# Optimization experiments

Hardware: AMD Instinct MI355X
Metric: run time of the kernel (lower is better)

The kernel has to match this reference:

```python
import jax, jax.numpy as jnp
import numpy as np

N = 100000          # nodes
E = 1600000         # edges (avg degree 16)
F_IN = 128          # input node features
H1, C1 = 8, 8       # conv1: 8 heads, 8 channels/head -> 64 concat
NUM_CLASSES = 40    # conv2: 1 head, 40 channels
EPS = 1e-16         # PyG softmax denominator epsilon
NEG_SLOPE = 0.2     # PyG GATConv default leaky_relu slope


def setup_inputs() -> dict:
    key = jax.random.key(0)
    ks = jax.random.split(key, 12)
    x = jax.random.normal(ks[0], (N, F_IN), jnp.float32)
    edge_index = jax.random.randint(ks[1], (2, E), 0, N, dtype=jnp.int64)
    edge_attr = jax.random.normal(ks[2], (E, 1), jnp.float32)
    # layer 1 params (Glorot-ish scaling)
    s1 = 1.0 / np.sqrt(F_IN)
    W1 = jax.random.normal(ks[3], (F_IN, H1 * C1), jnp.float32) * s1
    a_src1 = jax.random.normal(ks[4], (H1, C1), jnp.float32) * (1.0 / np.sqrt(C1))
    a_dst1 = jax.random.normal(ks[5], (H1, C1), jnp.float32) * (1.0 / np.sqrt(C1))
    b1 = jnp.zeros((H1 * C1,), jnp.float32)
    # layer 2 params: in = 64 (conv1 concat output), 1 head, NUM_CLASSES channels
    s2 = 1.0 / np.sqrt(H1 * C1)
    W2 = jax.random.normal(ks[6], (H1 * C1, NUM_CLASSES), jnp.float32) * s2
    a_src2 = jax.random.normal(ks[7], (1, NUM_CLASSES), jnp.float32) * (1.0 / np.sqrt(NUM_CLASSES))
    a_dst2 = jax.random.normal(ks[8], (1, NUM_CLASSES), jnp.float32) * (1.0 / np.sqrt(NUM_CLASSES))
    b2 = jnp.zeros((NUM_CLASSES,), jnp.float32)
    return {"x": x, "edge_index": edge_index, "edge_attr": edge_attr,
            "W1": W1, "a_src1": a_src1, "a_dst1": a_dst1, "b1": b1,
            "W2": W2, "a_src2": a_src2, "a_dst2": a_dst2, "b2": b2}


def gat_conv(x, src, dst, W, a_s, a_d, b, heads, out_ch):
    """PyG GATConv: linear -> per-edge leaky-relu attention -> dst softmax -> scatter-add."""
    n = x.shape[0]
    h = (x @ W).reshape(n, heads, out_ch)                 # [N,H,C]
    alpha_s = jnp.sum(h * a_s, axis=-1)                   # [N,H]
    alpha_d = jnp.sum(h * a_d, axis=-1)                   # [N,H]
    e = jax.nn.leaky_relu(alpha_s[src] + alpha_d[dst], NEG_SLOPE)  # [Etot,H]
    # segment softmax over incoming edges per destination node
    m = jax.ops.segment_max(e, dst, num_segments=n)       # [N,H]
    e = jnp.exp(e - m[dst])
    denom = jax.ops.segment_sum(e, dst, num_segments=n)   # [N,H]
    alpha = e / (denom[dst] + EPS)                        # [Etot,H]
    msg = h[src] * alpha[:, :, None]                      # [Etot,H,C]
    out = jax.ops.segment_sum(msg, dst, num_segments=n)   # [N,H,C]
    return out.reshape(n, heads * out_ch) + b             # concat heads + bias


def reference(x, edge_index, edge_attr, W1, a_src1, a_dst1, b1, W2, a_src2, a_dst2, b2):
    n = x.shape[0]
    # PyG GATConv adds self-loops by default
    loops = jnp.arange(n, dtype=edge_index.dtype)
    src = jnp.concatenate([edge_index[0], loops])
    dst = jnp.concatenate([edge_index[1], loops])
    x = x.astype(jnp.float32)
    x1 = jax.nn.elu(gat_conv(x, src, dst, W1, a_src1, a_dst1, b1, H1, C1))
    x2 = jax.nn.elu(gat_conv(x1, src, dst, W2, a_src2, a_dst2, b2, 1, NUM_CLASSES))
    return x2
```

## Files before the change

### kernel.cpp

```cpp
#include <hip/hip_runtime.h>
#include <math.h>

#define NN 100000
#define NE 1600000
#define NETOT (NE + NN)
#define FIN 128
#define H1N 8
#define D1 64
#define NC 40
#define LNT 64

#define BSH 9
#define BNODES 512
#define NBUC ((NN + BNODES - 1) / BNODES)
#define EPB 4096
#define NBLKA ((NE + EPB - 1) / EPB)
#define BCAP 9216

__device__ __forceinline__ float leakyf(float x) { return x >= 0.0f ? x : 0.2f * x; }
__device__ __forceinline__ float eluf(float x)   { return x > 0.0f ? x : expm1f(x); }

__device__ __forceinline__ unsigned short f2bf(float f) {
  unsigned u = __float_as_uint(f);
  u += 0x7fffu + ((u >> 16) & 1u);
  return (unsigned short)(u >> 16);
}
__device__ __forceinline__ float bf2f(unsigned short s) {
  return __uint_as_float((unsigned)s << 16);
}

__global__ void k_detect(const long long* __restrict__ ei, int* __restrict__ flag) {
  if (blockIdx.x == 0 && threadIdx.x == 0) {
    int is64 = 1;
    for (int i = 0; i < 16; ++i) {
      long long v = ei[i];
      if (v < 0 || v >= NN) is64 = 0;
    }
    *flag = is64;
  }
}

__global__ __launch_bounds__(256) void k_passA(const void* __restrict__ ei,
                        const int* __restrict__ flag,
                        unsigned int* __restrict__ subbuf, int* __restrict__ bcnt) {
  __shared__ unsigned int   pay[EPB];
  __shared__ unsigned short bk[EPB];
  __shared__ unsigned int   spay[EPB];
  __shared__ unsigned short sbk[EPB];
  __shared__ int hist[256];
  __shared__ int lstart[256];
  __shared__ int cur[256];
  __shared__ int gbase[256];
  int t = threadIdx.x;
  int e0 = blockIdx.x * EPB;
  int cnt = min(EPB, NE - e0);
  hist[t] = 0;
  __syncthreads();
  bool f64 = (*flag) != 0;
  for (int i = t; i < cnt; i += 256) {
    int s, d;
    if (f64) {
      const long long* p = (const long long*)ei;
      s = (int)p[e0 + i]; d = (int)p[NE + e0 + i];
    } else {
      const int* p = (const int*)ei;
      s = p[e0 + i]; d = p[NE + e0 + i];
    }
    int b = d >> BSH;
    pay[i] = ((unsigned)s << BSH) | (unsigned)(d & (BNODES - 1));
    bk[i] = (unsigned short)b;
    atomicAdd(&hist[b], 1);
  }
  __syncthreads();
  int v = hist[t];
  lstart[t] = v;
  __syncthreads();
  for (int st = 1; st < 256; st <<= 1) {
    int xv = (t >= st) ? lstart[t - st] : 0;
    __syncthreads();
    lstart[t] += xv;
    __syncthreads();
  }
  int excl = lstart[t] - v;
  __syncthreads();
  lstart[t] = excl;
  cur[t] = excl;
  gbase[t] = (v > 0) ? atomicAdd(&bcnt[t], v) : 0;
  __syncthreads();
  for (int i = t; i < cnt; i += 256) {
    int b = bk[i];
    int pos = atomicAdd(&cur[b], 1);
    spay[pos] = pay[i];
    sbk[pos] = (unsigned short)b;
  }
  __syncthreads();
  for (int i = t; i < cnt; i += 256) {
    int b = sbk[i];
    int o = gbase[b] + (i - lstart[b]);
    if (o < BCAP) subbuf[(size_t)b * BCAP + o] = spay[i];
  }
}

__global__ void k_bucketsum(const int* __restrict__ bcnt, int* __restrict__ bucket_base,
                            int* __restrict__ row_start) {
  __shared__ int sh[256];
  int t = threadIdx.x;
  int tot = 0;
  if (t < NBUC) {
    int d0 = t << BSH;
    int nloc = min(BNODES, NN - d0);
    tot = nloc + min(bcnt[t], BCAP);
  }
  sh[t] = tot;
  __syncthreads();
  for (int s = 1; s < 256; s <<= 1) {
    int x = (t >= s) ? sh[t - s] : 0;
    __syncthreads();
    sh[t] += x;
    __syncthreads();
  }
  if (t < NBUC) bucket_base[t] = sh[t] - tot;
  if (t == NBUC - 1) row_start[NN] = sh[t];
}

__global__ __launch_bounds__(256) void k_passB(const int* __restrict__ bcnt,
                       const unsigned int* __restrict__ subbuf,
                       const int* __restrict__ bucket_base,
                       int* __restrict__ row_start, int* __restrict__ csr) {
  __shared__ int hist[BNODES];
  __shared__ int ps[256];
  __shared__ int cur[BNODES];
  int b = blockIdx.x, t = threadIdx.x;
  int d0 = b << BSH;
  int nloc = min(BNODES, NN - d0);
  hist[t] = 0; hist[t + 256] = 0;
  __syncthreads();
  int cnt = min(bcnt[b], BCAP);
  const unsigned int* sb = subbuf + (size_t)b * BCAP;
  for (int i = t; i < cnt; i += 256)
    atomicAdd(&hist[sb[i] & (BNODES - 1)], 1);
  __syncthreads();
  int j0 = 2 * t, j1 = 2 * t + 1;
  int s0 = (j0 < nloc) ? hist[j0] + 1 : 0;
  int s1 = (j1 < nloc) ? hist[j1] + 1 : 0;
  int pairsum = s0 + s1;
  ps[t] = pairsum;
  __syncthreads();
  for (int s = 1; s < 256; s <<= 1) {
    int x = (t >= s) ? ps[t - s] : 0;
    __syncthreads();
    ps[t] += x;
    __syncthreads();
  }
  int excl = ps[t] - pairsum + bucket_base[b];
  if (j0 < nloc) {
    row_start[d0 + j0] = excl;
    csr[excl] = d0 + j0;
    cur[j0] = excl + 1;
  }
  if (j1 < nloc) {
    int rs = excl + s0;
    row_start[d0 + j1] = rs;
    csr[rs] = d0 + j1;
    cur[j1] = rs + 1;
  }
  __syncthreads();
  for (int i = t; i < cnt; i += 256) {
    unsigned u = sb[i];
    int pos = atomicAdd(&cur[u & (BNODES - 1)], 1);
    csr[pos] = (int)(u >> BSH);
  }
}

#define XS1(node, k) xs[(node) * FIN + ((k) ^ ((node) & 31))]
__global__ void k_lin1(const float* __restrict__ x, const float* __restrict__ W,
                       const float* __restrict__ aw_s, const float* __restrict__ aw_d,
                       unsigned short* __restrict__ h, float* __restrict__ als,
                       float* __restrict__ ald) {
  __shared__ float ws[FIN * D1];
  __shared__ float xs[LNT * FIN];
  int t = threadIdx.x;
  int base = blockIdx.x * LNT;
  for (int i = t; i < FIN * D1; i += 256) ws[i] = W[i];
  for (int i = t; i < LNT * FIN; i += 256) {
    int node = i >> 7, k = i & 127;
    int gn = base + node;
    if (gn >= NN) gn = NN - 1;
    XS1(node, k) = x[(size_t)gn * FIN + k];
  }
  __syncthreads();
  int head = t & 7, ng = t >> 3;
  int n0l = ng * 2, n1l = n0l + 1;
  float acc0[8] = {0, 0, 0, 0, 0, 0, 0, 0};
  float acc1[8] = {0, 0, 0, 0, 0, 0, 0, 0};
  #pragma unroll 4
  for (int k = 0; k < FIN; ++k) {
    float x0 = XS1(n0l, k);
    float x1v = XS1(n1l, k);
    const float4* wr = (const float4*)&ws[k * D1 + head * 8];
    float4 wa = wr[0], wb = wr[1];
    acc0[0] = fmaf(x0, wa.x, acc0[0]); acc1[0] = fmaf(x1v, wa.x, acc1[0]);
    acc0[1] = fmaf(x0, wa.y, acc0[1]); acc1[1] = fmaf(x1v, wa.y, acc1[1]);
    acc0[2] = fmaf(x0, wa.z, acc0[2]); acc1[2] = fmaf(x1v, wa.z, acc1[2]);
    acc0[3] = fmaf(x0, wa.w, acc0[3]); acc1[3] = fmaf(x1v, wa.w, acc1[3]);
    acc0[4] = fmaf(x0, wb.x, acc0[4]); acc1[4] = fmaf(x1v, wb.x, acc1[4]);
    acc0[5] = fmaf(x0, wb.y, acc0[5]); acc1[5] = fmaf(x1v, wb.y, acc1[5]);
    acc0[6] = fmaf(x0, wb.z, acc0[6]); acc1[6] = fmaf(x1v, wb.z, acc1[6]);
    acc0[7] = fmaf(x0, wb.w, acc0[7]); acc1[7] = fmaf(x1v, wb.w, acc1[7]);
  }
  int n0 = base + n0l, n1 = base + n1l;
  float aws[8], awd[8];
  #pragma unroll
  for (int c = 0; c < 8; ++c) { aws[c] = aw_s[head * 8 + c]; awd[c] = aw_d[head * 8 + c]; }
  if (n0 < NN) {
    float s = 0.f, d = 0.f;
    #pragma unroll
    for (int c = 0; c < 8; ++c) {
      h[(size_t)n0 * D1 + head * 8 + c] = f2bf(acc0[c]);
      s = fmaf(acc0[c], aws[c], s);
      d = fmaf(acc0[c], awd[c], d);
    }
    als[n0 * H1N + head] = s;
    ald[n0 * H1N + head] = d;
  }
  if (n1 < NN) {
    float s = 0.f, d = 0.f;
    #pragma unroll
    for (int c = 0; c < 8; ++c) {
      h[(size_t)n1 * D1 + head * 8 + c] = f2bf(acc1[c]);
      s = fmaf(acc1[c], aws[c], s);
      d = fmaf(acc1[c], awd[c], d);
    }
    als[n1 * H1N + head] = s;
    ald[n1 * H1N + head] = d;
  }
}

#define XS2(node, k) xs[(node) * D1 + ((k) ^ ((node) & 31))]
__global__ void k_lin2(const float* __restrict__ x, const float* __restrict__ W,
                       const float* __restrict__ aw_s, const float* __restrict__ aw_d,
                       unsigned short* __restrict__ h, float* __restrict__ als,
                       float* __restrict__ ald) {
  __shared__ float ws[D1 * D1];
  __shared__ float xs[LNT * D1];
  int t = threadIdx.x;
  int base = blockIdx.x * LNT;
  for (int i = t; i < D1 * D1; i += 256) {
    int k = i >> 6, c = i & 63;
    ws[i] = (c < NC) ? W[k * NC + c] : 0.f;
  }
  for (int i = t; i < LNT * D1; i += 256) {
    int node = i >> 6, k = i & 63;
    int gn = base + node;
    if (gn >= NN) gn = NN - 1;
    XS2(node, k) = x[(size_t)gn * D1 + k];
  }
  __syncthreads();
  int g = t & 7, ng = t >> 3;
  int n0l = ng * 2, n1l = n0l + 1;
  float acc0[8] = {0, 0, 0, 0, 0, 0, 0, 0};
  float acc1[8] = {0, 0, 0, 0, 0, 0, 0, 0};
  #pragma unroll 4
  for (int k = 0; k < D1; ++k) {
    float x0 = XS2(n0l, k);
    float x1v = XS2(n1l, k);
    const float4* wr = (const float4*)&ws[k * D1 + g * 8];
    float4 wa = wr[0], wb = wr[1];
    acc0[0] = fmaf(x0, wa.x, acc0[0]); acc1[0] = fmaf(x1v, wa.x, acc1[0]);
    acc0[1] = fmaf(x0, wa.y, acc0[1]); acc1[1] = fmaf(x1v, wa.y, acc1[1]);
    acc0[2] = fmaf(x0, wa.z, acc0[2]); acc1[2] = fmaf(x1v, wa.z, acc1[2]);
    acc0[3] = fmaf(x0, wa.w, acc0[3]); acc1[3] = fmaf(x1v, wa.w, acc1[3]);
    acc0[4] = fmaf(x0, wb.x, acc0[4]); acc1[4] = fmaf(x1v, wb.x, acc1[4]);
    acc0[5] = fmaf(x0, wb.y, acc0[5]); acc1[5] = fmaf(x1v, wb.y, acc1[5]);
    acc0[6] = fmaf(x0, wb.z, acc0[6]); acc1[6] = fmaf(x1v, wb.z, acc1[6]);
    acc0[7] = fmaf(x0, wb.w, acc0[7]); acc1[7] = fmaf(x1v, wb.w, acc1[7]);
  }
  int n0 = base + n0l, n1 = base + n1l;
  float aws[8], awd[8];
  #pragma unroll
  for (int c = 0; c < 8; ++c) {
    int col = g * 8 + c;
    aws[c] = (col < NC) ? aw_s[col] : 0.f;
    awd[c] = (col < NC) ? aw_d[col] : 0.f;
  }
  float s0 = 0.f, d0 = 0.f, s1 = 0.f, d1 = 0.f;
  #pragma unroll
  for (int c = 0; c < 8; ++c) {
    s0 = fmaf(acc0[c], aws[c], s0); d0 = fmaf(acc0[c], awd[c], d0);
    s1 = fmaf(acc1[c], aws[c], s1); d1 = fmaf(acc1[c], awd[c], d1);
  }
  s0 += __shfl_xor(s0, 1); d0 += __shfl_xor(d0, 1); s1 += __shfl_xor(s1, 1); d1 += __shfl_xor(d1, 1);
  s0 += __shfl_xor(s0, 2); d0 += __shfl_xor(d0, 2); s1 += __shfl_xor(s1, 2); d1 += __shfl_xor(d1, 2);
  s0 += __shfl_xor(s0, 4); d0 += __shfl_xor(d0, 4); s1 += __shfl_xor(s1, 4); d1 += __shfl_xor(d1, 4);
  if (n0 < NN && g < 5) {
    #pragma unroll
    for (int c = 0; c < 8; ++c) h[(size_t)n0 * NC + g * 8 + c] = f2bf(acc0[c]);
  }
  if (n1 < NN && g < 5) {
    #pragma unroll
    for (int c = 0; c < 8; ++c) h[(size_t)n1 * NC + g * 8 + c] = f2bf(acc1[c]);
  }
  if (g == 0) {
    if (n0 < NN) { als[n0] = s0; ald[n0] = d0; }
    if (n1 < NN) { als[n1] = s1; ald[n1] = d1; }
  }
}

__global__ void k_node1(const int* __restrict__ row_start, const int* __restrict__ csr,
                        const unsigned short* __restrict__ h, const float* __restrict__ als,
                        const float* __restrict__ ald, const float* __restrict__ b,
                        float* __restrict__ x1) {
  __shared__ float pl[4][64 * 9];
  int wid = threadIdx.x >> 6, lane = threadIdx.x & 63;
  int n = blockIdx.x * 4 + wid;
  if (n >= NN) return;
  float* pw = pl[wid];
  int r0 = row_start[n], r1 = row_start[n + 1];
  int hd = lane >> 3;
  const float4* adp = (const float4*)(ald + (size_t)n * H1N);
  float4 ad0 = adp[0], ad1 = adp[1];
  float S = 0.f, acc0 = 0.f, acc1 = 0.f, acc2 = 0.f, acc3 = 0.f;
  for (int kb = r0; kb < r1; kb += 64) {
    int cnt = min(64, r1 - kb);
    if (lane < cnt) {
      int sk = csr[kb + lane];
      const float4* ap = (const float4*)(als + (size_t)sk * H1N);
      float4 a0 = ap[0], a1 = ap[1];
      pw[lane * 9 + 0] = __expf(leakyf(a0.x + ad0.x));
      pw[lane * 9 + 1] = __expf(leakyf(a0.y + ad0.y));
      pw[lane * 9 + 2] = __expf(leakyf(a0.z + ad0.z));
      pw[lane * 9 + 3] = __expf(leakyf(a0.w + ad0.w));
      pw[lane * 9 + 4] = __expf(leakyf(a1.x + ad1.x));
      pw[lane * 9 + 5] = __expf(leakyf(a1.y + ad1.y));
      pw[lane * 9 + 6] = __expf(leakyf(a1.z + ad1.z));
      pw[lane * 9 + 7] = __expf(leakyf(a1.w + ad1.w));
      pw[lane * 9 + 8] = __int_as_float(sk);
    }
    asm volatile("s_waitcnt lgkmcnt(0)" ::: "memory");
    int j = 0;
    for (; j + 4 <= cnt; j += 4) {
      int s0 = __float_as_int(pw[(j + 0) * 9 + 8]);
      int s1 = __float_as_int(pw[(j + 1) * 9 + 8]);
      int s2 = __float_as_int(pw[(j + 2) * 9 + 8]);
      int s3 = __float_as_int(pw[(j + 3) * 9 + 8]);
      float p0 = pw[(j + 0) * 9 + hd], p1 = pw[(j + 1) * 9 + hd];
      float p2 = pw[(j + 2) * 9 + hd], p3 = pw[(j + 3) * 9 + hd];
      unsigned short u0 = h[(unsigned)s0 * D1 + lane];
      unsigned short u1 = h[(unsigned)s1 * D1 + lane];
      unsigned short u2 = h[(unsigned)s2 * D1 + lane];
      unsigned short u3 = h[(unsigned)s3 * D1 + lane];
      acc0 = fmaf(p0, bf2f(u0), acc0);
      acc1 = fmaf(p1, bf2f(u1), acc1);
      acc2 = fmaf(p2, bf2f(u2), acc2);
      acc3 = fmaf(p3, bf2f(u3), acc3);
      S += (p0 + p1) + (p2 + p3);
    }
    for (; j < cnt; ++j) {
      int s0 = __float_as_int(pw[j * 9 + 8]);
      float p0 = pw[j * 9 + hd];
      acc0 = fmaf(p0, bf2f(h[(unsigned)s0 * D1 + lane]), acc0);
      S += p0;
    }
  }
  float acc = (acc0 + acc1) + (acc2 + acc3);
  x1[(size_t)n * D1 + lane] = eluf(acc / (S + 1e-16f) + b[lane]);
}

__global__ void k_node2(const int* __restrict__ row_start, const int* __restrict__ csr,
                        const unsigned short* __restrict__ h, const float* __restrict__ als,
                        const float* __restrict__ ald, const float* __restrict__ b,
                        float* __restrict__ out) {
  __shared__ float pl[4][64 * 3];
  int wid = threadIdx.x >> 6, lane = threadIdx.x & 63;
  int n = blockIdx.x * 4 + wid;
  if (n >= NN) return;
  float* pw = pl[wid];
  int r0 = row_start[n], r1 = row_start[n + 1];
  int cl = lane < NC ? lane : NC - 1;
  float aldn = ald[n];
  float S = 0.f, acc0 = 0.f, acc1 = 0.f, acc2 = 0.f, acc3 = 0.f;
  for (int kb = r0; kb < r1; kb += 64) {
    int cnt = min(64, r1 - kb);
    if (lane < cnt) {
      int sk = csr[kb + lane];
      pw[lane * 3 + 0] = __expf(leakyf(als[sk] + aldn));
      pw[lane * 3 + 1] = __int_as_float(sk);
    }
    asm volatile("s_waitcnt lgkmcnt(0)" ::: "memory");
    int j = 0;
    for (; j + 4 <= cnt; j += 4) {
      int s0 = __float_as_int(pw[(j + 0) * 3 + 1]);
      int s1 = __float_as_int(pw[(j + 1) * 3 + 1]);
      int s2 = __float_as_int(pw[(j + 2) * 3 + 1]);
      int s3 = __float_as_int(pw[(j + 3) * 3 + 1]);
      float p0 = pw[(j + 0) * 3], p1 = pw[(j + 1) * 3];
      float p2 = pw[(j + 2) * 3], p3 = pw[(j + 3) * 3];
      unsigned short u0 = h[(unsigned)s0 * NC + cl];
      unsigned short u1 = h[(unsigned)s1 * NC + cl];
      unsigned short u2 = h[(unsigned)s2 * NC + cl];
      unsigned short u3 = h[(unsigned)s3 * NC + cl];
      acc0 = fmaf(p0, bf2f(u0), acc0);
      acc1 = fmaf(p1, bf2f(u1), acc1);
      acc2 = fmaf(p2, bf2f(u2), acc2);
      acc3 = fmaf(p3, bf2f(u3), acc3);
      S += (p0 + p1) + (p2 + p3);
    }
    for (; j < cnt; ++j) {
      int s0 = __float_as_int(pw[j * 3 + 1]);
      float p0 = pw[j * 3];
      acc0 = fmaf(p0, bf2f(h[(unsigned)s0 * NC + cl]), acc0);
      S += p0;
    }
  }
  float acc = (acc0 + acc1) + (acc2 + acc3);
  if (lane < NC) out[(size_t)n * NC + lane] = eluf(acc / (S + 1e-16f) + b[lane]);
}

extern "C" void kernel_launch(void* const* d_in, const int* in_sizes, int n_in,
                              void* d_out, int out_size, void* d_ws, size_t ws_size,
                              hipStream_t stream) {
  const float* x    = (const float*)d_in[0];
  const void*  ei   = d_in[1];
  const float* W1   = (const float*)d_in[3];
  const float* as1w = (const float*)d_in[4];
  const float* ad1w = (const float*)d_in[5];
  const float* b1   = (const float*)d_in[6];
  const float* W2   = (const float*)d_in[7];
  const float* as2w = (const float*)d_in[8];
  const float* ad2w = (const float*)d_in[9];
  const float* b2   = (const float*)d_in[10];
  float* out = (float*)d_out;

  char* w = (char*)d_ws;
  size_t off = 0;
  auto carve = [&](size_t bytes) -> void* {
    void* r = w + off;
    off += (bytes + 255) & ~(size_t)255;
    return r;
  };
  int*            flag        = (int*)carve(256);
  int*            bcnt        = (int*)carve((size_t)NBUC * 4);
  int*            bucket_base = (int*)carve((size_t)NBUC * 4);
  unsigned int*   subbuf      = (unsigned int*)carve((size_t)NBUC * BCAP * 4);
  int*            row_start   = (int*)carve((size_t)(NN + 1) * 4);
  int*            csr         = (int*)carve((size_t)NETOT * 4);
  unsigned short* h1          = (unsigned short*)carve((size_t)NN * D1 * 2);
  float*          als1        = (float*)carve((size_t)NN * H1N * 4);
  float*          ald1        = (float*)carve((size_t)NN * H1N * 4);
  float*          x1          = (float*)carve((size_t)NN * D1 * 4);
  unsigned short* h2 = h1; float* als2 = als1; float* ald2 = ald1;

  const int LB = (NN + LNT - 1) / LNT;

  k_detect<<<1, 64, 0, stream>>>((const long long*)ei, flag);
  hipMemsetAsync(bcnt, 0, (size_t)NBUC * 4, stream);
  k_passA<<<NBLKA, 256, 0, stream>>>(ei, flag, subbuf, bcnt);
  k_bucketsum<<<1, 256, 0, stream>>>(bcnt, bucket_base, row_start);
  k_passB<<<NBUC, 256, 0, stream>>>(bcnt, subbuf, bucket_base, row_start, csr);

  k_lin1<<<LB, 256, 0, stream>>>(x, W1, as1w, ad1w, h1, als1, ald1);
  k_node1<<<NN / 4, 256, 0, stream>>>(row_start, csr, h1, als1, ald1, b1, x1);

  k_lin2<<<LB, 256, 0, stream>>>(x1, W2, as2w, ad2w, h2, als2, ald2);
  k_node2<<<NN / 4, 256, 0, stream>>>(row_start, csr, h2, als2, ald2, b2, out);
}
```

Measured before the change: 243.4 us.

## Process two nodes per wavefront with packed bf16 pairs and exp2 attention

Node aggregation kernels now assign a half-wave (32 lanes) per node, each lane handling two packed bf16 channels via 32-bit gathers, which halves the wave count and lane waste for the 40-class layer. Attention logits are prescaled by log2(e) in the linear kernels so the softmax uses the hardware exp2 instruction. The intermediate layer-1 output is stored as packed bf16 instead of fp32, cutting write and read traffic for the second linear kernel. This adds extra bf16 rounding of x1 and wider per-lane accumulator state.

```diff
diff --git a/kernel.cpp b/kernel.cpp
--- a/kernel.cpp
+++ b/kernel.cpp
@@ -9,6 +9,7 @@
 #define D1 64
 #define NC 40
 #define LNT 64
+#define LOG2E 1.44269504088896f
 
 #define BSH 9
 #define BNODES 512
@@ -19,15 +20,15 @@
 
 __device__ __forceinline__ float leakyf(float x) { return x >= 0.0f ? x : 0.2f * x; }
 __device__ __forceinline__ float eluf(float x)   { return x > 0.0f ? x : expm1f(x); }
+__device__ __forceinline__ float exp2fast(float x) { return __builtin_amdgcn_exp2f(x); }
 
 __device__ __forceinline__ unsigned short f2bf(float f) {
   unsigned u = __float_as_uint(f);
   u += 0x7fffu + ((u >> 16) & 1u);
   return (unsigned short)(u >> 16);
 }
-__device__ __forceinline__ float bf2f(unsigned short s) {
-  return __uint_as_float((unsigned)s << 16);
-}
+__device__ __forceinline__ float bflo(unsigned u) { return __uint_as_float(u << 16); }
+__device__ __forceinline__ float bfhi(unsigned u) { return __uint_as_float(u & 0xffff0000u); }
 
 __global__ void k_detect(const long long* __restrict__ ei, int* __restrict__ flag) {
   if (blockIdx.x == 0 && threadIdx.x == 0) {
@@ -220,8 +221,8 @@
       s = fmaf(acc0[c], aws[c], s);
       d = fmaf(acc0[c], awd[c], d);
     }
-    als[n0 * H1N + head] = s;
-    ald[n0 * H1N + head] = d;
+    als[n0 * H1N + head] = s * LOG2E;
+    ald[n0 * H1N + head] = d * LOG2E;
   }
   if (n1 < NN) {
     float s = 0.f, d = 0.f;
@@ -231,13 +232,13 @@
       s = fmaf(acc1[c], aws[c], s);
       d = fmaf(acc1[c], awd[c], d);
     }
-    als[n1 * H1N + head] = s;
-    ald[n1 * H1N + head] = d;
+    als[n1 * H1N + head] = s * LOG2E;
+    ald[n1 * H1N + head] = d * LOG2E;
   }
 }
 
 #define XS2(node, k) xs[(node) * D1 + ((k) ^ ((node) & 31))]
-__global__ void k_lin2(const float* __restrict__ x, const float* __restrict__ W,
+__global__ void k_lin2(const unsigned int* __restrict__ x1bf, const float* __restrict__ W,
                        const float* __restrict__ aw_s, const float* __restrict__ aw_d,
                        unsigned short* __restrict__ h, float* __restrict__ als,
                        float* __restrict__ ald) {
@@ -249,11 +250,13 @@
     int k = i >> 6, c = i & 63;
     ws[i] = (c < NC) ? W[k * NC + c] : 0.f;
   }
-  for (int i = t; i < LNT * D1; i += 256) {
-    int node = i >> 6, k = i & 63;
+  for (int i = t; i < LNT * 32; i += 256) {
+    int node = i >> 5, kd = i & 31;
     int gn = base + node;
     if (gn >= NN) gn = NN - 1;
-    XS2(node, k) = x[(size_t)gn * D1 + k];
+    unsigned u = x1bf[(size_t)gn * 32 + kd];
+    XS2(node, 2 * kd)     = bflo(u);
+    XS2(node, 2 * kd + 1) = bfhi(u);
   }
   __syncthreads();
   int g = t & 7, ng = t >> 3;
@@ -301,40 +304,42 @@
     for (int c = 0; c < 8; ++c) h[(size_t)n1 * NC + g * 8 + c] = f2bf(acc1[c]);
   }
   if (g == 0) {
-    if (n0 < NN) { als[n0] = s0; ald[n0] = d0; }
-    if (n1 < NN) { als[n1] = s1; ald[n1] = d1; }
+    if (n0 < NN) { als[n0] = s0 * LOG2E; ald[n0] = d0 * LOG2E; }
+    if (n1 < NN) { als[n1] = s1 * LOG2E; ald[n1] = d1 * LOG2E; }
   }
 }
 
 __global__ void k_node1(const int* __restrict__ row_start, const int* __restrict__ csr,
                         const unsigned short* __restrict__ h, const float* __restrict__ als,
                         const float* __restrict__ ald, const float* __restrict__ b,
-                        float* __restrict__ x1) {
-  __shared__ float pl[4][64 * 9];
-  int wid = threadIdx.x >> 6, lane = threadIdx.x & 63;
-  int n = blockIdx.x * 4 + wid;
-  if (n >= NN) return;
-  float* pw = pl[wid];
+                        unsigned int* __restrict__ x1bf) {
+  __shared__ float pl[4][2][32 * 9];
+  int wid = threadIdx.x >> 6, half = (threadIdx.x >> 5) & 1, c2 = threadIdx.x & 31;
+  int n = blockIdx.x * 8 + wid * 2 + half;
+  float* pw = pl[wid][half];
+  const unsigned int* h32 = (const unsigned int*)h;
   int r0 = row_start[n], r1 = row_start[n + 1];
-  int hd = lane >> 3;
+  int hd = c2 >> 2;
   const float4* adp = (const float4*)(ald + (size_t)n * H1N);
   float4 ad0 = adp[0], ad1 = adp[1];
-  float S = 0.f, acc0 = 0.f, acc1 = 0.f, acc2 = 0.f, acc3 = 0.f;
-  for (int kb = r0; kb < r1; kb += 64) {
-    int cnt = min(64, r1 - kb);
-    if (lane < cnt) {
-      int sk = csr[kb + lane];
+  float S = 0.f;
+  float alo0 = 0.f, ahi0 = 0.f, alo1 = 0.f, ahi1 = 0.f;
+  float alo2 = 0.f, ahi2 = 0.f, alo3 = 0.f, ahi3 = 0.f;
+  for (int kb = r0; kb < r1; kb += 32) {
+    int cnt = min(32, r1 - kb);
+    if (c2 < cnt) {
+      int sk = csr[kb + c2];
       const float4* ap = (const float4*)(als + (size_t)sk * H1N);
       float4 a0 = ap[0], a1 = ap[1];
-      pw[lane * 9 + 0] = __expf(leakyf(a0.x + ad0.x));
-      pw[lane * 9 + 1] = __expf(leakyf(a0.y + ad0.y));
-      pw[lane * 9 + 2] = __expf(leakyf(a0.z + ad0.z));
-      pw[lane * 9 + 3] = __expf(leakyf(a0.w + ad0.w));
-      pw[lane * 9 + 4] = __expf(leakyf(a1.x + ad1.x));
-      pw[lane * 9 + 5] = __expf(leakyf(a1.y + ad1.y));
-      pw[lane * 9 + 6] = __expf(leakyf(a1.z + ad1.z));
-      pw[lane * 9 + 7] = __expf(leakyf(a1.w + ad1.w));
-      pw[lane * 9 + 8] = __int_as_float(sk);
+      pw[c2 * 9 + 0] = exp2fast(leakyf(a0.x + ad0.x));
+      pw[c2 * 9 + 1] = exp2fast(leakyf(a0.y + ad0.y));
+      pw[c2 * 9 + 2] = exp2fast(leakyf(a0.z + ad0.z));
+      pw[c2 * 9 + 3] = exp2fast(leakyf(a0.w + ad0.w));
+      pw[c2 * 9 + 4] = exp2fast(leakyf(a1.x + ad1.x));
+      pw[c2 * 9 + 5] = exp2fast(leakyf(a1.y + ad1.y));
+      pw[c2 * 9 + 6] = exp2fast(leakyf(a1.z + ad1.z));
+      pw[c2 * 9 + 7] = exp2fast(leakyf(a1.w + ad1.w));
+      pw[c2 * 9 + 8] = __int_as_float(sk);
     }
     asm volatile("s_waitcnt lgkmcnt(0)" ::: "memory");
     int j = 0;
@@ -345,46 +350,53 @@
       int s3 = __float_as_int(pw[(j + 3) * 9 + 8]);
       float p0 = pw[(j + 0) * 9 + hd], p1 = pw[(j + 1) * 9 + hd];
       float p2 = pw[(j + 2) * 9 + hd], p3 = pw[(j + 3) * 9 + hd];
-      unsigned short u0 = h[(unsigned)s0 * D1 + lane];
-      unsigned short u1 = h[(unsigned)s1 * D1 + lane];
-      unsigned short u2 = h[(unsigned)s2 * D1 + lane];
-      unsigned short u3 = h[(unsigned)s3 * D1 + lane];
-      acc0 = fmaf(p0, bf2f(u0), acc0);
-      acc1 = fmaf(p1, bf2f(u1), acc1);
-      acc2 = fmaf(p2, bf2f(u2), acc2);
-      acc3 = fmaf(p3, bf2f(u3), acc3);
+      unsigned u0 = h32[(unsigned)s0 * 32 + c2];
+      unsigned u1 = h32[(unsigned)s1 * 32 + c2];
+      unsigned u2 = h32[(unsigned)s2 * 32 + c2];
+      unsigned u3 = h32[(unsigned)s3 * 32 + c2];
+      alo0 = fmaf(p0, bflo(u0), alo0); ahi0 = fmaf(p0, bfhi(u0), ahi0);
+      alo1 = fmaf(p1, bflo(u1), alo1); ahi1 = fmaf(p1, bfhi(u1), ahi1);
+      alo2 = fmaf(p2, bflo(u2), alo2); ahi2 = fmaf(p2, bfhi(u2), ahi2);
+      alo3 = fmaf(p3, bflo(u3), alo3); ahi3 = fmaf(p3, bfhi(u3), ahi3);
       S += (p0 + p1) + (p2 + p3);
     }
     for (; j < cnt; ++j) {
       int s0 = __float_as_int(pw[j * 9 + 8]);
       float p0 = pw[j * 9 + hd];
-      acc0 = fmaf(p0, bf2f(h[(unsigned)s0 * D1 + lane]), acc0);
+      unsigned u0 = h32[(unsigned)s0 * 32 + c2];
+      alo0 = fmaf(p0, bflo(u0), alo0); ahi0 = fmaf(p0, bfhi(u0), ahi0);
       S += p0;
     }
   }
-  float acc = (acc0 + acc1) + (acc2 + acc3);
-  x1[(size_t)n * D1 + lane] = eluf(acc / (S + 1e-16f) + b[lane]);
+  float alo = (alo0 + alo1) + (alo2 + alo3);
+  float ahi = (ahi0 + ahi1) + (ahi2 + ahi3);
+  float inv = 1.0f / (S + 1e-16f);
+  float ox = eluf(alo * inv + b[2 * c2 + 0]);
+  float oy = eluf(ahi * inv + b[2 * c2 + 1]);
+  x1bf[(size_t)n * 32 + c2] = (unsigned)f2bf(ox) | ((unsigned)f2bf(oy) << 16);
 }
 
 __global__ void k_node2(const int* __restrict__ row_start, const int* __restrict__ csr,
                         const unsigned short* __restrict__ h, const float* __restrict__ als,
                         const float* __restrict__ ald, const float* __restrict__ b,
                         float* __restrict__ out) {
-  __shared__ float pl[4][64 * 3];
-  int wid = threadIdx.x >> 6, lane = threadIdx.x & 63;
-  int n = blockIdx.x * 4 + wid;
-  if (n >= NN) return;
-  float* pw = pl[wid];
+  __shared__ float pl[4][2][32 * 3];
+  int wid = threadIdx.x >> 6, half = (threadIdx.x >> 5) & 1, c2 = threadIdx.x & 31;
+  int n = blockIdx.x * 8 + wid * 2 + half;
+  float* pw = pl[wid][half];
+  const unsigned int* h32 = (const unsigned int*)h;
   int r0 = row_start[n], r1 = row_start[n + 1];
-  int cl = lane < NC ? lane : NC - 1;
+  int cl = c2 < 20 ? c2 : 19;
   float aldn = ald[n];
-  float S = 0.f, acc0 = 0.f, acc1 = 0.f, acc2 = 0.f, acc3 = 0.f;
-  for (int kb = r0; kb < r1; kb += 64) {
-    int cnt = min(64, r1 - kb);
-    if (lane < cnt) {
-      int sk = csr[kb + lane];
-      pw[lane * 3 + 0] = __expf(leakyf(als[sk] + aldn));
-      pw[lane * 3 + 1] = __int_as_float(sk);
+  float S = 0.f;
+  float alo0 = 0.f, ahi0 = 0.f, alo1 = 0.f, ahi1 = 0.f;
+  float alo2 = 0.f, ahi2 = 0.f, alo3 = 0.f, ahi3 = 0.f;
+  for (int kb = r0; kb < r1; kb += 32) {
+    int cnt = min(32, r1 - kb);
+    if (c2 < cnt) {
+      int sk = csr[kb + c2];
+      pw[c2 * 3 + 0] = exp2fast(leakyf(als[sk] + aldn));
+      pw[c2 * 3 + 1] = __int_as_float(sk);
     }
     asm volatile("s_waitcnt lgkmcnt(0)" ::: "memory");
     int j = 0;
@@ -395,25 +407,33 @@
       int s3 = __float_as_int(pw[(j + 3) * 3 + 1]);
       float p0 = pw[(j + 0) * 3], p1 = pw[(j + 1) * 3];
       float p2 = pw[(j + 2) * 3], p3 = pw[(j + 3) * 3];
-      unsigned short u0 = h[(unsigned)s0 * NC + cl];
-      unsigned short u1 = h[(unsigned)s1 * NC + cl];
-      unsigned short u2 = h[(unsigned)s2 * NC + cl];
-      unsigned short u3 = h[(unsigned)s3 * NC + cl];
-      acc0 = fmaf(p0, bf2f(u0), acc0);
-      acc1 = fmaf(p1, bf2f(u1), acc1);
-      acc2 = fmaf(p2, bf2f(u2), acc2);
-      acc3 = fmaf(p3, bf2f(u3), acc3);
+      unsigned u0 = h32[(unsigned)s0 * 20 + cl];
+      unsigned u1 = h32[(unsigned)s1 * 20 + cl];
+      unsigned u2 = h32[(unsigned)s2 * 20 + cl];
+      unsigned u3 = h32[(unsigned)s3 * 20 + cl];
+      alo0 = fmaf(p0, bflo(u0), alo0); ahi0 = fmaf(p0, bfhi(u0), ahi0);
+      alo1 = fmaf(p1, bflo(u1), alo1); ahi1 = fmaf(p1, bfhi(u1), ahi1);
+      alo2 = fmaf(p2, bflo(u2), alo2); ahi2 = fmaf(p2, bfhi(u2), ahi2);
+      alo3 = fmaf(p3, bflo(u3), alo3); ahi3 = fmaf(p3, bfhi(u3), ahi3);
       S += (p0 + p1) + (p2 + p3);
     }
     for (; j < cnt; ++j) {
       int s0 = __float_as_int(pw[j * 3 + 1]);
       float p0 = pw[j * 3];
-      acc0 = fmaf(p0, bf2f(h[(unsigned)s0 * NC + cl]), acc0);
+      unsigned u0 = h32[(unsigned)s0 * 20 + cl];
+      alo0 = fmaf(p0, bflo(u0), alo0); ahi0 = fmaf(p0, bfhi(u0), ahi0);
       S += p0;
     }
   }
-  float acc = (acc0 + acc1) + (acc2 + acc3);
-  if (lane < NC) out[(size_t)n * NC + lane] = eluf(acc / (S + 1e-16f) + b[lane]);
+  float alo = (alo0 + alo1) + (alo2 + alo3);
+  float ahi = (ahi0 + ahi1) + (ahi2 + ahi3);
+  if (c2 < 20) {
+    float inv = 1.0f / (S + 1e-16f);
+    float2 o;
+    o.x = eluf(alo * inv + b[2 * c2 + 0]);
+    o.y = eluf(ahi * inv + b[2 * c2 + 1]);
+    ((float2*)out)[(size_t)n * 20 + c2] = o;
+  }
 }
 
 extern "C" void kernel_launch(void* const* d_in, const int* in_sizes, int n_in,
@@ -447,20 +467,20 @@
   unsigned short* h1          = (unsigned short*)carve((size_t)NN * D1 * 2);
   float*          als1        = (float*)carve((size_t)NN * H1N * 4);
   float*          ald1        = (float*)carve((size_t)NN * H1N * 4);
-  float*          x1          = (float*)carve((size_t)NN * D1 * 4);
+  unsigned int*   x1bf        = (unsigned int*)carve((size_t)NN * 32 * 4);
   unsigned short* h2 = h1; float* als2 = als1; float* ald2 = ald1;
 
   const int LB = (NN + LNT - 1) / LNT;
 
   k_detect<<<1, 64, 0, stream>>>((const long long*)ei, flag);
-  hipMemsetAsync(bcnt, 0, (size_t)NBUC * 4, stream);
+  (void)hipMemsetAsync(bcnt, 0, (size_t)NBUC * 4, stream);
   k_passA<<<NBLKA, 256, 0, stream>>>(ei, flag, subbuf, bcnt);
   k_bucketsum<<<1, 256, 0, stream>>>(bcnt, bucket_base, row_start);
   k_passB<<<NBUC, 256, 0, stream>>>(bcnt, subbuf, bucket_base, row_start, csr);
 
   k_lin1<<<LB, 256, 0, stream>>>(x, W1, as1w, ad1w, h1, als1, ald1);
-  k_node1<<<NN / 4, 256, 0, stream>>>(row_start, csr, h1, als1, ald1, b1, x1);
-
-  k_lin2<<<LB, 256, 0, stream>>>(x1, W2, as2w, ad2w, h2, als2, ald2);
-  k_node2<<<NN / 4, 256, 0, stream>>>(row_start, csr, h2, als2, ald2, b2, out);
-}
+  k_node1<<<NN / 8, 256, 0, stream>>>(row_start, csr, h1, als1, ald1, b1, x1bf);
+
+  k_lin2<<<LB, 256, 0, stream>>>(x1bf, W2, as2w, ad2w, h2, als2, ald2);
+  k_node2<<<NN / 8, 256, 0, stream>>>(row_start, csr, h2, als2, ald2, b2, out);
+}
```

Result: faster. 217.8 us (-10.5%).
